# Performance work log

Hardware: AMD Instinct MI355X
Metric: run time of the kernel (lower is better)

The kernel has to match this reference:

```python
import jax, jax.numpy as jnp
import numpy as np
import math

B, S, D, H = 4, 2048, 512, 8
HD = D // H  # head dim = 64

def setup_inputs() -> dict:
    key = jax.random.key(0)
    ks = jax.random.split(key, 12)
    inp = {
        'queries': jax.random.normal(ks[0], (B, S, D), jnp.float32),
        'keys': jax.random.normal(ks[1], (B, S, D), jnp.float32),
        'values': jax.random.normal(ks[2], (B, S, D), jnp.float32),
        'valid_lens': jax.random.randint(ks[3], (B,), 0, 2048, jnp.int32),
        'Wq': jax.random.normal(ks[4], (D, D), jnp.float32) / math.sqrt(D),
        'bq': jnp.zeros((D,), jnp.float32),
        'Wk': jax.random.normal(ks[5], (D, D), jnp.float32) / math.sqrt(D),
        'bk': jnp.zeros((D,), jnp.float32),
        'Wv': jax.random.normal(ks[6], (D, D), jnp.float32) / math.sqrt(D),
        'bv': jnp.zeros((D,), jnp.float32),
        'Wo': jax.random.normal(ks[7], (D, D), jnp.float32) / math.sqrt(D),
        'bo': jnp.zeros((D,), jnp.float32),
    }
    return inp

def reference(queries, keys, values, valid_lens, Wq, bq, Wk, bk, Wv, bv, Wo, bo):
    # project and split heads: [B,S,D] -> [B,H,S,HD]
    def split_heads(x):
        return x.reshape(B, S, H, HD).transpose(0, 2, 1, 3)
    q = split_heads(queries @ Wq + bq)
    k = split_heads(keys @ Wk + bk)
    v = split_heads(values @ Wv + bv)
    # scores [B,H,Sq,Sk]
    scores = jnp.einsum('bhqd,bhkd->bhqk', q, k) / math.sqrt(HD)
    # masked softmax: mask key positions >= valid_len with -1e6 (d2l semantics)
    mask = jnp.arange(S)[None, None, None, :] < valid_lens[:, None, None, None]
    scores = jnp.where(mask, scores, -1e6)
    attn = jax.nn.softmax(scores, axis=-1)
    out = jnp.einsum('bhqk,bhkd->bhqd', attn, v)  # [B,H,S,HD]
    out = out.transpose(0, 2, 1, 3).reshape(B, S, D)
    return out @ Wo + bo
```

## Files before the change

### kernel.cpp

```cpp
#include <hip/hip_runtime.h>
#include <hip/hip_bf16.h>

typedef _Float16 half8 __attribute__((ext_vector_type(8)));
typedef _Float16 half4 __attribute__((ext_vector_type(4)));
typedef float floatx4 __attribute__((ext_vector_type(4)));
typedef float floatx16 __attribute__((ext_vector_type(16)));
typedef unsigned int uint2v __attribute__((ext_vector_type(2)));

#define LOG2E 1.44269504088896340736f

__device__ __forceinline__ half8 cvt8r(floatx4 a, floatx4 b) {
    half8 h;
    h[0] = (_Float16)a[0]; h[1] = (_Float16)a[1]; h[2] = (_Float16)a[2]; h[3] = (_Float16)a[3];
    h[4] = (_Float16)b[0]; h[5] = (_Float16)b[1]; h[6] = (_Float16)b[2]; h[7] = (_Float16)b[3];
    return h;
}

union H8U { half8 h; uint2v u[2]; };

__global__ __launch_bounds__(256) void transpose_w_kernel(
        const float* __restrict__ Wq, const float* __restrict__ Wk,
        const float* __restrict__ Wv, const float* __restrict__ Wo,
        _Float16* __restrict__ out) {
    const float* W = (blockIdx.z == 0) ? Wq : (blockIdx.z == 1) ? Wk : (blockIdx.z == 2) ? Wv : Wo;
    _Float16* o = out + (size_t)blockIdx.z * 512 * 512;
    __shared__ __align__(16) _Float16 t[64][72];
    int r0 = blockIdx.x * 64, c0 = blockIdx.y * 64;
    int tid = threadIdx.x;
    for (int i = 0; i < 2; i++) {
        int f = i * 256 + tid;
        int row = f >> 3, seg = f & 7;
        const float* p = W + (size_t)(r0 + row) * 512 + c0 + seg * 8;
        *(half8*)&t[row][seg * 8] = cvt8r(*(const floatx4*)p, *(const floatx4*)(p + 4));
    }
    __syncthreads();
    for (int i = 0; i < 2; i++) {
        int f = i * 256 + tid;
        int crow = f >> 3, seg = f & 7;
        half8 hv;
        for (int j = 0; j < 8; j++) hv[j] = t[seg * 8 + j][crow];
        *(half8*)(o + (size_t)(c0 + crow) * 512 + r0 + seg * 8) = hv;
    }
}

__global__ __launch_bounds__(256) void gemm_qkv_kernel(
        const float* __restrict__ Xq, const float* __restrict__ Xk, const float* __restrict__ Xv,
        const _Float16* __restrict__ WTall,
        const float* __restrict__ bq, const float* __restrict__ bk, const float* __restrict__ bv,
        const int* __restrict__ vlens,
        _Float16* __restrict__ qo, _Float16* __restrict__ ko2, _Float16* __restrict__ vto) {
    int z = blockIdx.z;
    int mBase = blockIdx.x * 64, nBase = blockIdx.y * 128;

    if (z >= 1) {
        int b_ = mBase >> 11, s0 = mBase & 2047;
        int L = vlens[b_];
        if (s0 >= L && !(z == 2 && L == 0)) return;
    }

    const float* X = (z == 0) ? Xq : (z == 1) ? Xk : Xv;
    const _Float16* BT = WTall + (size_t)z * 512 * 512;
    const float* bias = (z == 0) ? bq : (z == 1) ? bk : bv;

    __shared__ __align__(16) _Float16 Asm[64][72];
    __shared__ __align__(16) _Float16 Bsm[128][72];

    int tid = threadIdx.x;
    int wave = tid >> 6, lane = tid & 63;
    int lrow = lane & 15, quad = lane >> 4;
    int mrow = wave * 16 + lrow;

    const floatx4 fz = {0.f, 0.f, 0.f, 0.f};
    floatx4 acc[8];
    for (int i = 0; i < 8; i++) acc[i] = fz;

    int arow[2], aseg[2], brow[4], bseg[4];
    for (int i = 0; i < 2; i++) { int f = i * 256 + tid; arow[i] = f >> 3; aseg[i] = f & 7; }
    for (int i = 0; i < 4; i++) { int f = i * 256 + tid; brow[i] = f >> 3; bseg[i] = f & 7; }

    floatx4 areg[2][2];
    half8 breg[4];
    for (int i = 0; i < 2; i++) {
        const float* pa = X + (size_t)(mBase + arow[i]) * 512 + aseg[i] * 8;
        areg[i][0] = *(const floatx4*)pa;
        areg[i][1] = *(const floatx4*)(pa + 4);
    }
    for (int i = 0; i < 4; i++)
        breg[i] = *(const half8*)(BT + (size_t)(nBase + brow[i]) * 512 + bseg[i] * 8);

    for (int kb = 0; kb < 512; kb += 64) {
        for (int i = 0; i < 2; i++) *(half8*)&Asm[arow[i]][aseg[i] * 8] = cvt8r(areg[i][0], areg[i][1]);
        for (int i = 0; i < 4; i++) *(half8*)&Bsm[brow[i]][bseg[i] * 8] = breg[i];
        __syncthreads();
        if (kb + 64 < 512) {
            int kn = kb + 64;
            for (int i = 0; i < 2; i++) {
                const float* pa = X + (size_t)(mBase + arow[i]) * 512 + kn + aseg[i] * 8;
                areg[i][0] = *(const floatx4*)pa;
                areg[i][1] = *(const floatx4*)(pa + 4);
            }
            for (int i = 0; i < 4; i++)
                breg[i] = *(const half8*)(BT + (size_t)(nBase + brow[i]) * 512 + kn + bseg[i] * 8);
        }
        for (int kc = 0; kc < 2; kc++) {
            int ko_ = kc * 32 + quad * 8;
            half8 a = *(const half8*)&Asm[mrow][ko_];
            for (int nt = 0; nt < 8; nt++) {
                half8 b = *(const half8*)&Bsm[nt * 16 + lrow][ko_];
                acc[nt] = __builtin_amdgcn_mfma_f32_16x16x32_f16(a, b, acc[nt], 0, 0, 0);
            }
        }
        __syncthreads();
    }

    if (z == 2) {
        for (int nt = 0; nt < 8; nt++) {
            int gc = nBase + nt * 16 + lrow;
            float bb = bias[gc];
            int h = gc >> 6, hd = gc & 63;
            int gr = mBase + wave * 16 + quad * 4;
            int b_ = gr >> 11, s = gr & 2047;
            half4 hv;
            for (int r = 0; r < 4; r++) hv[r] = (_Float16)(acc[nt][r] + bb);
            *(half4*)(vto + (((size_t)(b_ * 8 + h) * 64 + hd) * 2048 + s)) = hv;
        }
    } else {
        _Float16* out = (z == 0) ? qo : ko2;
        for (int nt = 0; nt < 8; nt++) {
            int gc = nBase + nt * 16 + lrow;
            float bb = bias[gc];
            int h = gc >> 6, hd = gc & 63;
            for (int r = 0; r < 4; r++) {
                int gr = mBase + wave * 16 + quad * 4 + r;
                int b_ = gr >> 11, s = gr & 2047;
                out[(((size_t)b_ * 8 + h) * 2048 + s) * 64 + hd] = (_Float16)(acc[nt][r] + bb);
            }
        }
    }
}

__global__ __launch_bounds__(128) void attn_kernel(
        const _Float16* __restrict__ qws, const _Float16* __restrict__ kws,
        const _Float16* __restrict__ vtws, const int* __restrict__ vlens,
        _Float16* __restrict__ aout) {
    int idx = blockIdx.x;
    int b = ((idx & 3) + (idx >> 8)) & 3;
    int h = (idx >> 2) & 7;
    int q0 = ((idx >> 5) & 31) * 64;
    int bh = b * 8 + h;
    int L = vlens[b];
    bool uni = (L == 0);
    int nkt = uni ? 32 : ((L + 63) >> 6);
    int nfull = uni ? 0 : (L >> 6);

    int tid = threadIdx.x;
    int wq = tid >> 6;
    int lane = tid & 63;
    int l31 = lane & 31, hi = lane >> 5;

    __shared__ __align__(16) _Float16 ksm[64 * 64];
    __shared__ __align__(16) _Float16 vtsm[64 * 64];
    char* ksmB = (char*)ksm;
    char* vsmB = (char*)vtsm;

    const _Float16* kbase = kws + (size_t)bh * 2048 * 64;
    const _Float16* vtbase = vtws + (size_t)bh * 64 * 2048;

    half8 qf[4];
    {
        const _Float16* qrow = qws + ((size_t)bh * 2048 + q0 + wq * 32 + l31) * 64;
#pragma unroll
        for (int kc = 0; kc < 4; kc++) {
            qf[kc] = *(const half8*)(qrow + kc * 16 + hi * 8);
            qf[kc] = qf[kc] * (_Float16)(0.125f * LOG2E);
        }
    }

    floatx16 oacc0, oacc1;
#pragma unroll
    for (int i = 0; i < 16; i++) { oacc0[i] = 0.f; oacc1[i] = 0.f; }
    float rs = 0.f;

    int seg = tid & 7;
    int trow = tid >> 3;
    int xr = (l31 & 15) << 3;

    half8 kreg[4], vreg[4];
#pragma unroll
    for (int i = 0; i < 4; i++) {
        int row = i * 16 + trow;
        kreg[i] = *(const half8*)(kbase + row * 64 + seg * 8);
        vreg[i] = *(const half8*)(vtbase + (size_t)row * 2048 + seg * 8);
    }

    for (int kt = 0; kt < nkt; kt++) {
#pragma unroll
        for (int i = 0; i < 4; i++) {
            int row = i * 16 + trow;
            int wo = row * 128 + ((seg * 16) ^ ((row & 15) << 3));
            H8U kv, vv;
            kv.h = kreg[i]; vv.h = vreg[i];
            *(uint2v*)(ksmB + wo) = kv.u[0];
            *(uint2v*)(ksmB + (wo ^ 8)) = kv.u[1];
            *(uint2v*)(vsmB + wo) = vv.u[0];
            *(uint2v*)(vsmB + (wo ^ 8)) = vv.u[1];
        }
        __syncthreads();
        if (kt + 1 < nkt) {
            const _Float16* kn = kbase + (size_t)(kt + 1) * 4096;
            const _Float16* vn = vtbase + (kt + 1) * 64;
#pragma unroll
            for (int i = 0; i < 4; i++) {
                int row = i * 16 + trow;
                kreg[i] = *(const half8*)(kn + row * 64 + seg * 8);
                vreg[i] = *(const half8*)(vn + (size_t)row * 2048 + seg * 8);
            }
        }

#pragma unroll
        for (int t = 0; t < 2; t++) {
            floatx16 sacc;
#pragma unroll
            for (int i = 0; i < 16; i++) sacc[i] = 0.f;
            int rbase = (t * 32 + l31) * 128;
#pragma unroll
            for (int kc = 0; kc < 4; kc++) {
                int off = rbase + ((kc * 32 + hi * 16) ^ xr);
                H8U kf;
                kf.u[0] = *(const uint2v*)(ksmB + off);
                kf.u[1] = *(const uint2v*)(ksmB + (off ^ 8));
                sacc = __builtin_amdgcn_mfma_f32_32x32x16_f16(kf.h, qf[kc], sacc, 0, 0, 0);
            }

            float p[16];
            if (kt < nfull) {
#pragma unroll
                for (int r = 0; r < 16; r++) p[r] = exp2f(sacc[r]);
            } else {
                int kb0 = kt * 64 + t * 32 + 4 * hi;
#pragma unroll
                for (int r = 0; r < 16; r++) {
                    int key = kb0 + (r & 3) + 8 * (r >> 2);
                    p[r] = uni ? 1.0f : ((key < L) ? exp2f(sacc[r]) : 0.0f);
                }
            }
#pragma unroll
            for (int r = 0; r < 16; r++) rs += p[r];

#pragma unroll
            for (int s2 = 0; s2 < 2; s2++) {
                int s = t * 2 + s2;
                H8U pa;
#pragma unroll
                for (int j = 0; j < 8; j++) pa.h[j] = (_Float16)p[s2 * 8 + j];
                int cb = (s * 32 + hi * 8) ^ xr;
                {
                    int off = l31 * 128 + cb;
                    H8U vf;
                    vf.u[0] = *(const uint2v*)(vsmB + off);
                    vf.u[1] = *(const uint2v*)(vsmB + (off ^ 16));
                    oacc0 = __builtin_amdgcn_mfma_f32_32x32x16_f16(pa.h, vf.h, oacc0, 0, 0, 0);
                }
                {
                    int off = (32 + l31) * 128 + cb;
                    H8U vf;
                    vf.u[0] = *(const uint2v*)(vsmB + off);
                    vf.u[1] = *(const uint2v*)(vsmB + (off ^ 16));
                    oacc1 = __builtin_amdgcn_mfma_f32_32x32x16_f16(pa.h, vf.h, oacc1, 0, 0, 0);
                }
            }
        }
        __syncthreads();
    }

    float rstot = rs + __shfl_xor(rs, 32, 64);
    _Float16* outb = aout + ((size_t)b * 2048 + q0 + wq * 32) * 512 + h * 64;
#pragma unroll
    for (int r = 0; r < 16; r++) {
        int qi = (r & 3) + 8 * (r >> 2) + 4 * hi;
        float inv = 1.0f / __shfl(rstot, qi, 64);
        outb[(size_t)qi * 512 + l31] = (_Float16)(oacc0[r] * inv);
        outb[(size_t)qi * 512 + 32 + l31] = (_Float16)(oacc1[r] * inv);
    }
}

__global__ __launch_bounds__(256) void gemm_out_kernel(
        const _Float16* __restrict__ A, const _Float16* __restrict__ BT,
        const float* __restrict__ bias, float* __restrict__ out) {
    __shared__ __align__(16) _Float16 Asm[64][72];
    __shared__ __align__(16) _Float16 Bsm[128][72];

    int tid = threadIdx.x;
    int wave = tid >> 6, lane = tid & 63;
    int lrow = lane & 15, quad = lane >> 4;
    int mBase = blockIdx.x * 64, nBase = blockIdx.y * 128;
    int mrow = wave * 16 + lrow;

    const floatx4 fz = {0.f, 0.f, 0.f, 0.f};
    floatx4 acc[8];
    for (int i = 0; i < 8; i++) acc[i] = fz;

    int arow[2], aseg[2], brow[4], bseg[4];
    for (int i = 0; i < 2; i++) { int f = i * 256 + tid; arow[i] = f >> 3; aseg[i] = f & 7; }
    for (int i = 0; i < 4; i++) { int f = i * 256 + tid; brow[i] = f >> 3; bseg[i] = f & 7; }

    half8 areg[2], breg[4];
    for (int i = 0; i < 2; i++)
        areg[i] = *(const half8*)(A + (size_t)(mBase + arow[i]) * 512 + aseg[i] * 8);
    for (int i = 0; i < 4; i++)
        breg[i] = *(const half8*)(BT + (size_t)(nBase + brow[i]) * 512 + bseg[i] * 8);

    for (int kb = 0; kb < 512; kb += 64) {
        for (int i = 0; i < 2; i++) *(half8*)&Asm[arow[i]][aseg[i] * 8] = areg[i];
        for (int i = 0; i < 4; i++) *(half8*)&Bsm[brow[i]][bseg[i] * 8] = breg[i];
        __syncthreads();
        if (kb + 64 < 512) {
            int kn = kb + 64;
            for (int i = 0; i < 2; i++)
                areg[i] = *(const half8*)(A + (size_t)(mBase + arow[i]) * 512 + kn + aseg[i] * 8);
            for (int i = 0; i < 4; i++)
                breg[i] = *(const half8*)(BT + (size_t)(nBase + brow[i]) * 512 + kn + bseg[i] * 8);
        }
        for (int kc = 0; kc < 2; kc++) {
            int ko_ = kc * 32 + quad * 8;
            half8 a = *(const half8*)&Asm[mrow][ko_];
            for (int nt = 0; nt < 8; nt++) {
                half8 b = *(const half8*)&Bsm[nt * 16 + lrow][ko_];
                acc[nt] = __builtin_amdgcn_mfma_f32_16x16x32_f16(a, b, acc[nt], 0, 0, 0);
            }
        }
        __syncthreads();
    }

    for (int nt = 0; nt < 8; nt++) {
        int gc = nBase + nt * 16 + lrow;
        float bb = bias[gc];
        for (int r = 0; r < 4; r++) {
            int gr = mBase + wave * 16 + quad * 4 + r;
            out[(size_t)gr * 512 + gc] = acc[nt][r] + bb;
        }
    }
}

extern "C" void kernel_launch(void* const* d_in, const int* in_sizes, int n_in,
                              void* d_out, int out_size, void* d_ws, size_t ws_size,
                              hipStream_t stream) {
    const float* Q  = (const float*)d_in[0];
    const float* K  = (const float*)d_in[1];
    const float* V  = (const float*)d_in[2];
    const int*   VL = (const int*)d_in[3];
    const float* Wq = (const float*)d_in[4];
    const float* bq = (const float*)d_in[5];
    const float* Wk = (const float*)d_in[6];
    const float* bk = (const float*)d_in[7];
    const float* Wv = (const float*)d_in[8];
    const float* bv = (const float*)d_in[9];
    const float* Wo = (const float*)d_in[10];
    const float* bo = (const float*)d_in[11];

    char* ws = (char*)d_ws;
    _Float16* WT   = (_Float16*)ws;
    _Float16* qws  = (_Float16*)(ws + (size_t)(2)  * 1024 * 1024);
    _Float16* kws  = (_Float16*)(ws + (size_t)(10) * 1024 * 1024);
    _Float16* aout = (_Float16*)(ws + (size_t)(18) * 1024 * 1024);
    _Float16* vtws = (_Float16*)(ws + (size_t)(26) * 1024 * 1024);

    transpose_w_kernel<<<dim3(8, 8, 4), 256, 0, stream>>>(Wq, Wk, Wv, Wo, WT);
    gemm_qkv_kernel<<<dim3(128, 4, 3), 256, 0, stream>>>(Q, K, V, WT, bq, bk, bv, VL, qws, kws, vtws);
    attn_kernel<<<dim3(1024, 1, 1), 128, 0, stream>>>(qws, kws, vtws, VL, aout);
    gemm_out_kernel<<<dim3(128, 4, 1), 256, 0, stream>>>(aout, WT + (size_t)3 * 512 * 512, bo, (float*)d_out);
}
```

Baseline: 194.0 us.

## Double attention key tile to 128 with new LDS swizzle and packed conversions

The attention kernel now stages 128 keys per iteration instead of 64, which halves the number of barrier-separated loop trips. It also switches to a new XOR swizzle so K fragments load as single 16-byte LDS reads. P is converted with packed cvt_pkrtz, 32-key sub-tiles entirely beyond the valid length are skipped, and the row sums use tree reduction into two partial accumulators. In exchange it uses twice the LDS and twice the prefetch registers per block, which may lower occupancy.

```diff
diff --git a/kernel.cpp b/kernel.cpp
--- a/kernel.cpp
+++ b/kernel.cpp
@@ -3,6 +3,7 @@
 
 typedef _Float16 half8 __attribute__((ext_vector_type(8)));
 typedef _Float16 half4 __attribute__((ext_vector_type(4)));
+typedef _Float16 half2t __attribute__((ext_vector_type(2)));
 typedef float floatx4 __attribute__((ext_vector_type(4)));
 typedef float floatx16 __attribute__((ext_vector_type(16)));
 typedef unsigned int uint2v __attribute__((ext_vector_type(2)));
@@ -16,7 +17,11 @@
     return h;
 }
 
-union H8U { half8 h; uint2v u[2]; };
+union H8U { half8 h; half2t v2[4]; uint2v u[2]; };
+
+__device__ __forceinline__ half2t pk16(float a, float b) {
+    return __builtin_bit_cast(half2t, __builtin_amdgcn_cvt_pkrtz(a, b));
+}
 
 __global__ __launch_bounds__(256) void transpose_w_kernel(
         const float* __restrict__ Wq, const float* __restrict__ Wk,
@@ -150,16 +155,16 @@
     int bh = b * 8 + h;
     int L = vlens[b];
     bool uni = (L == 0);
-    int nkt = uni ? 32 : ((L + 63) >> 6);
-    int nfull = uni ? 0 : (L >> 6);
+    int nkt = uni ? 16 : ((L + 127) >> 7);
+    int nfull = uni ? 0 : (L >> 7);
 
     int tid = threadIdx.x;
     int wq = tid >> 6;
     int lane = tid & 63;
     int l31 = lane & 31, hi = lane >> 5;
 
-    __shared__ __align__(16) _Float16 ksm[64 * 64];
-    __shared__ __align__(16) _Float16 vtsm[64 * 64];
+    __shared__ __align__(16) _Float16 ksm[128 * 64];
+    __shared__ __align__(16) _Float16 vtsm[64 * 128];
     char* ksmB = (char*)ksm;
     char* vsmB = (char*)vtsm;
 
@@ -176,60 +181,54 @@
         }
     }
 
-    floatx16 oacc0, oacc1;
-#pragma unroll
-    for (int i = 0; i < 16; i++) { oacc0[i] = 0.f; oacc1[i] = 0.f; }
-    float rs = 0.f;
-
-    int seg = tid & 7;
-    int trow = tid >> 3;
-    int xr = (l31 & 15) << 3;
-
-    half8 kreg[4], vreg[4];
-#pragma unroll
-    for (int i = 0; i < 4; i++) {
-        int row = i * 16 + trow;
-        kreg[i] = *(const half8*)(kbase + row * 64 + seg * 8);
-        vreg[i] = *(const half8*)(vtbase + (size_t)row * 2048 + seg * 8);
+    floatx16 oc0, oc1;
+#pragma unroll
+    for (int i = 0; i < 16; i++) { oc0[i] = 0.f; oc1[i] = 0.f; }
+    float rsp0 = 0.f, rsp1 = 0.f;
+
+    int kthr = tid >> 3, ksg = tid & 7;
+    int vthr = tid >> 4, vsg = tid & 15;
+    int x15 = l31 & 15, x7 = l31 & 7;
+
+    half8 kreg[8], vreg[8];
+#pragma unroll
+    for (int i = 0; i < 8; i++) {
+        kreg[i] = *(const half8*)(kbase + (i * 16 + kthr) * 64 + ksg * 8);
+        vreg[i] = *(const half8*)(vtbase + (size_t)(i * 8 + vthr) * 2048 + vsg * 8);
     }
 
     for (int kt = 0; kt < nkt; kt++) {
 #pragma unroll
-        for (int i = 0; i < 4; i++) {
-            int row = i * 16 + trow;
-            int wo = row * 128 + ((seg * 16) ^ ((row & 15) << 3));
-            H8U kv, vv;
-            kv.h = kreg[i]; vv.h = vreg[i];
-            *(uint2v*)(ksmB + wo) = kv.u[0];
-            *(uint2v*)(ksmB + (wo ^ 8)) = kv.u[1];
-            *(uint2v*)(vsmB + wo) = vv.u[0];
-            *(uint2v*)(vsmB + (wo ^ 8)) = vv.u[1];
+        for (int i = 0; i < 8; i++) {
+            int kr = i * 16 + kthr;
+            *(half8*)(ksmB + kr * 128 + ((ksg ^ (kr & 7)) << 4)) = kreg[i];
+            int vr = i * 8 + vthr;
+            *(half8*)(vsmB + vr * 256 + ((vsg ^ (vr & 15)) << 4)) = vreg[i];
         }
         __syncthreads();
         if (kt + 1 < nkt) {
-            const _Float16* kn = kbase + (size_t)(kt + 1) * 4096;
-            const _Float16* vn = vtbase + (kt + 1) * 64;
-#pragma unroll
-            for (int i = 0; i < 4; i++) {
-                int row = i * 16 + trow;
-                kreg[i] = *(const half8*)(kn + row * 64 + seg * 8);
-                vreg[i] = *(const half8*)(vn + (size_t)row * 2048 + seg * 8);
-            }
-        }
-
-#pragma unroll
-        for (int t = 0; t < 2; t++) {
+            const _Float16* kn = kbase + (size_t)(kt + 1) * 128 * 64;
+            const _Float16* vn = vtbase + (kt + 1) * 128;
+#pragma unroll
+            for (int i = 0; i < 8; i++) {
+                kreg[i] = *(const half8*)(kn + (i * 16 + kthr) * 64 + ksg * 8);
+                vreg[i] = *(const half8*)(vn + (size_t)(i * 8 + vthr) * 2048 + vsg * 8);
+            }
+        }
+
+#pragma unroll
+        for (int t = 0; t < 4; t++) {
+            if (!uni && kt * 128 + t * 32 >= L) continue;
+
             floatx16 sacc;
 #pragma unroll
             for (int i = 0; i < 16; i++) sacc[i] = 0.f;
             int rbase = (t * 32 + l31) * 128;
 #pragma unroll
             for (int kc = 0; kc < 4; kc++) {
-                int off = rbase + ((kc * 32 + hi * 16) ^ xr);
-                H8U kf;
-                kf.u[0] = *(const uint2v*)(ksmB + off);
-                kf.u[1] = *(const uint2v*)(ksmB + (off ^ 8));
-                sacc = __builtin_amdgcn_mfma_f32_32x32x16_f16(kf.h, qf[kc], sacc, 0, 0, 0);
+                int c = 2 * kc + hi;
+                half8 kf = *(const half8*)(ksmB + rbase + ((c ^ x7) << 4));
+                sacc = __builtin_amdgcn_mfma_f32_32x32x16_f16(kf, qf[kc], sacc, 0, 0, 0);
             }
 
             float p[16];
@@ -237,50 +236,48 @@
 #pragma unroll
                 for (int r = 0; r < 16; r++) p[r] = exp2f(sacc[r]);
             } else {
-                int kb0 = kt * 64 + t * 32 + 4 * hi;
+                int kb0 = kt * 128 + t * 32 + 4 * hi;
 #pragma unroll
                 for (int r = 0; r < 16; r++) {
                     int key = kb0 + (r & 3) + 8 * (r >> 2);
                     p[r] = uni ? 1.0f : ((key < L) ? exp2f(sacc[r]) : 0.0f);
                 }
             }
-#pragma unroll
-            for (int r = 0; r < 16; r++) rs += p[r];
+            float ts = (((p[0] + p[1]) + (p[2] + p[3])) + ((p[4] + p[5]) + (p[6] + p[7])))
+                     + (((p[8] + p[9]) + (p[10] + p[11])) + ((p[12] + p[13]) + (p[14] + p[15])));
+            if (t & 1) rsp1 += ts; else rsp0 += ts;
 
 #pragma unroll
             for (int s2 = 0; s2 < 2; s2++) {
                 int s = t * 2 + s2;
                 H8U pa;
 #pragma unroll
-                for (int j = 0; j < 8; j++) pa.h[j] = (_Float16)p[s2 * 8 + j];
-                int cb = (s * 32 + hi * 8) ^ xr;
-                {
-                    int off = l31 * 128 + cb;
-                    H8U vf;
-                    vf.u[0] = *(const uint2v*)(vsmB + off);
-                    vf.u[1] = *(const uint2v*)(vsmB + (off ^ 16));
-                    oacc0 = __builtin_amdgcn_mfma_f32_32x32x16_f16(pa.h, vf.h, oacc0, 0, 0, 0);
-                }
-                {
-                    int off = (32 + l31) * 128 + cb;
-                    H8U vf;
-                    vf.u[0] = *(const uint2v*)(vsmB + off);
-                    vf.u[1] = *(const uint2v*)(vsmB + (off ^ 16));
-                    oacc1 = __builtin_amdgcn_mfma_f32_32x32x16_f16(pa.h, vf.h, oacc1, 0, 0, 0);
-                }
-            }
-        }
-        __syncthreads();
-    }
-
+                for (int jj = 0; jj < 4; jj++)
+                    pa.v2[jj] = pk16(p[s2 * 8 + jj * 2], p[s2 * 8 + jj * 2 + 1]);
+                int cA = (((2 * s) ^ x15) << 4) + 8 * hi;
+                int cB = (((2 * s + 1) ^ x15) << 4) + 8 * hi;
+                int ro0 = l31 * 256, ro1 = (32 + l31) * 256;
+                H8U vf0, vf1;
+                vf0.u[0] = *(const uint2v*)(vsmB + ro0 + cA);
+                vf0.u[1] = *(const uint2v*)(vsmB + ro0 + cB);
+                vf1.u[0] = *(const uint2v*)(vsmB + ro1 + cA);
+                vf1.u[1] = *(const uint2v*)(vsmB + ro1 + cB);
+                oc0 = __builtin_amdgcn_mfma_f32_32x32x16_f16(pa.h, vf0.h, oc0, 0, 0, 0);
+                oc1 = __builtin_amdgcn_mfma_f32_32x32x16_f16(pa.h, vf1.h, oc1, 0, 0, 0);
+            }
+        }
+        __syncthreads();
+    }
+
+    float rs = rsp0 + rsp1;
     float rstot = rs + __shfl_xor(rs, 32, 64);
     _Float16* outb = aout + ((size_t)b * 2048 + q0 + wq * 32) * 512 + h * 64;
 #pragma unroll
     for (int r = 0; r < 16; r++) {
         int qi = (r & 3) + 8 * (r >> 2) + 4 * hi;
         float inv = 1.0f / __shfl(rstot, qi, 64);
-        outb[(size_t)qi * 512 + l31] = (_Float16)(oacc0[r] * inv);
-        outb[(size_t)qi * 512 + 32 + l31] = (_Float16)(oacc1[r] * inv);
+        outb[(size_t)qi * 512 + l31] = (_Float16)(oc0[r] * inv);
+        outb[(size_t)qi * 512 + 32 + l31] = (_Float16)(oc1[r] * inv);
     }
 }
 
```

New measurement: 195.4 us. No clear change (+0.7%).

## Split attention key tiles across two wave pairs with LDS reduction

Applied to the files above, without the earlier changes.

The attention block grows from 128 to 256 threads. Each pair of waves processes alternating 64-key tiles, with each half of the block loading its own tile into a separate LDS buffer. The two partial output accumulators and row sums are then combined through shared memory before normalization. This doubles the waves working on each query block so latency is better hidden, at the cost of twice the LDS, an extra reduction step, and wasted work when the number of tiles is odd. The unused half2 union member appears to be leftover.

```diff
diff --git a/kernel.cpp b/kernel.cpp
--- a/kernel.cpp
+++ b/kernel.cpp
@@ -3,6 +3,7 @@
 
 typedef _Float16 half8 __attribute__((ext_vector_type(8)));
 typedef _Float16 half4 __attribute__((ext_vector_type(4)));
+typedef _Float16 half2t __attribute__((ext_vector_type(2)));
 typedef float floatx4 __attribute__((ext_vector_type(4)));
 typedef float floatx16 __attribute__((ext_vector_type(16)));
 typedef unsigned int uint2v __attribute__((ext_vector_type(2)));
@@ -16,7 +17,7 @@
     return h;
 }
 
-union H8U { half8 h; uint2v u[2]; };
+union H8U { half8 h; half2t v2[4]; uint2v u[2]; };
 
 __global__ __launch_bounds__(256) void transpose_w_kernel(
         const float* __restrict__ Wq, const float* __restrict__ Wk,
@@ -139,7 +140,7 @@
     }
 }
 
-__global__ __launch_bounds__(128) void attn_kernel(
+__global__ __launch_bounds__(256) void attn_kernel(
         const _Float16* __restrict__ qws, const _Float16* __restrict__ kws,
         const _Float16* __restrict__ vtws, const int* __restrict__ vlens,
         _Float16* __restrict__ aout) {
@@ -154,14 +155,13 @@
     int nfull = uni ? 0 : (L >> 6);
 
     int tid = threadIdx.x;
-    int wq = tid >> 6;
+    int wid = tid >> 6;
+    int wq = wid & 1, ks = wid >> 1;
     int lane = tid & 63;
     int l31 = lane & 31, hi = lane >> 5;
 
-    __shared__ __align__(16) _Float16 ksm[64 * 64];
-    __shared__ __align__(16) _Float16 vtsm[64 * 64];
-    char* ksmB = (char*)ksm;
-    char* vsmB = (char*)vtsm;
+    __shared__ __align__(16) _Float16 ksm[2][64 * 64];
+    __shared__ __align__(16) _Float16 vtsm[2][64 * 64];
 
     const _Float16* kbase = kws + (size_t)bh * 2048 * 64;
     const _Float16* vtbase = vtws + (size_t)bh * 64 * 2048;
@@ -181,106 +181,140 @@
     for (int i = 0; i < 16; i++) { oacc0[i] = 0.f; oacc1[i] = 0.f; }
     float rs = 0.f;
 
-    int seg = tid & 7;
-    int trow = tid >> 3;
+    int htid = tid & 127;
+    int tt = tid >> 7;
+    int seg = htid & 7;
+    int trow = htid >> 3;
     int xr = (l31 & 15) << 3;
+    char* ksmB = (char*)&ksm[tt][0];
+    char* vsmB = (char*)&vtsm[tt][0];
 
     half8 kreg[4], vreg[4];
-#pragma unroll
-    for (int i = 0; i < 4; i++) {
-        int row = i * 16 + trow;
-        kreg[i] = *(const half8*)(kbase + row * 64 + seg * 8);
-        vreg[i] = *(const half8*)(vtbase + (size_t)row * 2048 + seg * 8);
-    }
-
-    for (int kt = 0; kt < nkt; kt++) {
+    if (tt < nkt) {
+        const _Float16* kp = kbase + (size_t)tt * 4096;
+        const _Float16* vp = vtbase + tt * 64;
 #pragma unroll
         for (int i = 0; i < 4; i++) {
             int row = i * 16 + trow;
-            int wo = row * 128 + ((seg * 16) ^ ((row & 15) << 3));
-            H8U kv, vv;
-            kv.h = kreg[i]; vv.h = vreg[i];
-            *(uint2v*)(ksmB + wo) = kv.u[0];
-            *(uint2v*)(ksmB + (wo ^ 8)) = kv.u[1];
-            *(uint2v*)(vsmB + wo) = vv.u[0];
-            *(uint2v*)(vsmB + (wo ^ 8)) = vv.u[1];
-        }
-        __syncthreads();
-        if (kt + 1 < nkt) {
-            const _Float16* kn = kbase + (size_t)(kt + 1) * 4096;
-            const _Float16* vn = vtbase + (kt + 1) * 64;
+            kreg[i] = *(const half8*)(kp + row * 64 + seg * 8);
+            vreg[i] = *(const half8*)(vp + (size_t)row * 2048 + seg * 8);
+        }
+    }
+
+    for (int kt2 = 0; kt2 < nkt; kt2 += 2) {
+        if (kt2 + tt < nkt) {
 #pragma unroll
             for (int i = 0; i < 4; i++) {
                 int row = i * 16 + trow;
-                kreg[i] = *(const half8*)(kn + row * 64 + seg * 8);
-                vreg[i] = *(const half8*)(vn + (size_t)row * 2048 + seg * 8);
-            }
-        }
-
-#pragma unroll
-        for (int t = 0; t < 2; t++) {
-            floatx16 sacc;
-#pragma unroll
-            for (int i = 0; i < 16; i++) sacc[i] = 0.f;
-            int rbase = (t * 32 + l31) * 128;
-#pragma unroll
-            for (int kc = 0; kc < 4; kc++) {
-                int off = rbase + ((kc * 32 + hi * 16) ^ xr);
-                H8U kf;
-                kf.u[0] = *(const uint2v*)(ksmB + off);
-                kf.u[1] = *(const uint2v*)(ksmB + (off ^ 8));
-                sacc = __builtin_amdgcn_mfma_f32_32x32x16_f16(kf.h, qf[kc], sacc, 0, 0, 0);
-            }
-
-            float p[16];
-            if (kt < nfull) {
-#pragma unroll
-                for (int r = 0; r < 16; r++) p[r] = exp2f(sacc[r]);
-            } else {
-                int kb0 = kt * 64 + t * 32 + 4 * hi;
-#pragma unroll
-                for (int r = 0; r < 16; r++) {
-                    int key = kb0 + (r & 3) + 8 * (r >> 2);
-                    p[r] = uni ? 1.0f : ((key < L) ? exp2f(sacc[r]) : 0.0f);
+                int wo = row * 128 + ((seg * 16) ^ ((row & 15) << 3));
+                H8U kv, vv;
+                kv.h = kreg[i]; vv.h = vreg[i];
+                *(uint2v*)(ksmB + wo) = kv.u[0];
+                *(uint2v*)(ksmB + (wo ^ 8)) = kv.u[1];
+                *(uint2v*)(vsmB + wo) = vv.u[0];
+                *(uint2v*)(vsmB + (wo ^ 8)) = vv.u[1];
+            }
+        }
+        __syncthreads();
+        int nxt = kt2 + 2 + tt;
+        if (nxt < nkt) {
+            const _Float16* kp = kbase + (size_t)nxt * 4096;
+            const _Float16* vp = vtbase + nxt * 64;
+#pragma unroll
+            for (int i = 0; i < 4; i++) {
+                int row = i * 16 + trow;
+                kreg[i] = *(const half8*)(kp + row * 64 + seg * 8);
+                vreg[i] = *(const half8*)(vp + (size_t)row * 2048 + seg * 8);
+            }
+        }
+
+        int kt = kt2 + ks;
+        if (kt < nkt) {
+#pragma unroll
+            for (int t = 0; t < 2; t++) {
+                floatx16 sacc;
+#pragma unroll
+                for (int i = 0; i < 16; i++) sacc[i] = 0.f;
+                int rbase = (t * 32 + l31) * 128;
+#pragma unroll
+                for (int kc = 0; kc < 4; kc++) {
+                    int off = rbase + ((kc * 32 + hi * 16) ^ xr);
+                    H8U kf;
+                    kf.u[0] = *(const uint2v*)(ksmB + off);
+                    kf.u[1] = *(const uint2v*)(ksmB + (off ^ 8));
+                    sacc = __builtin_amdgcn_mfma_f32_32x32x16_f16(kf.h, qf[kc], sacc, 0, 0, 0);
                 }
-            }
-#pragma unroll
-            for (int r = 0; r < 16; r++) rs += p[r];
-
-#pragma unroll
-            for (int s2 = 0; s2 < 2; s2++) {
-                int s = t * 2 + s2;
-                H8U pa;
-#pragma unroll
-                for (int j = 0; j < 8; j++) pa.h[j] = (_Float16)p[s2 * 8 + j];
-                int cb = (s * 32 + hi * 8) ^ xr;
-                {
-                    int off = l31 * 128 + cb;
-                    H8U vf;
-                    vf.u[0] = *(const uint2v*)(vsmB + off);
-                    vf.u[1] = *(const uint2v*)(vsmB + (off ^ 16));
-                    oacc0 = __builtin_amdgcn_mfma_f32_32x32x16_f16(pa.h, vf.h, oacc0, 0, 0, 0);
+
+                float p[16];
+                if (kt < nfull) {
+#pragma unroll
+                    for (int r = 0; r < 16; r++) p[r] = exp2f(sacc[r]);
+                } else {
+                    int kb0 = kt * 64 + t * 32 + 4 * hi;
+#pragma unroll
+                    for (int r = 0; r < 16; r++) {
+                        int key = kb0 + (r & 3) + 8 * (r >> 2);
+                        p[r] = uni ? 1.0f : ((key < L) ? exp2f(sacc[r]) : 0.0f);
+                    }
                 }
-                {
-                    int off = (32 + l31) * 128 + cb;
-                    H8U vf;
-                    vf.u[0] = *(const uint2v*)(vsmB + off);
-                    vf.u[1] = *(const uint2v*)(vsmB + (off ^ 16));
-                    oacc1 = __builtin_amdgcn_mfma_f32_32x32x16_f16(pa.h, vf.h, oacc1, 0, 0, 0);
+#pragma unroll
+                for (int r = 0; r < 16; r++) rs += p[r];
+
+#pragma unroll
+                for (int s2 = 0; s2 < 2; s2++) {
+                    int s = t * 2 + s2;
+                    H8U pa;
+#pragma unroll
+                    for (int j = 0; j < 8; j++) pa.h[j] = (_Float16)p[s2 * 8 + j];
+                    int cb = (s * 32 + hi * 8) ^ xr;
+                    {
+                        int off = l31 * 128 + cb;
+                        H8U vf;
+                        vf.u[0] = *(const uint2v*)(vsmB + off);
+                        vf.u[1] = *(const uint2v*)(vsmB + (off ^ 16));
+                        oacc0 = __builtin_amdgcn_mfma_f32_32x32x16_f16(pa.h, vf.h, oacc0, 0, 0, 0);
+                    }
+                    {
+                        int off = (32 + l31) * 128 + cb;
+                        H8U vf;
+                        vf.u[0] = *(const uint2v*)(vsmB + off);
+                        vf.u[1] = *(const uint2v*)(vsmB + (off ^ 16));
+                        oacc1 = __builtin_amdgcn_mfma_f32_32x32x16_f16(pa.h, vf.h, oacc1, 0, 0, 0);
+                    }
                 }
             }
         }
         __syncthreads();
     }
 
-    float rstot = rs + __shfl_xor(rs, 32, 64);
-    _Float16* outb = aout + ((size_t)b * 2048 + q0 + wq * 32) * 512 + h * 64;
-#pragma unroll
-    for (int r = 0; r < 16; r++) {
-        int qi = (r & 3) + 8 * (r >> 2) + 4 * hi;
-        float inv = 1.0f / __shfl(rstot, qi, 64);
-        outb[(size_t)qi * 512 + l31] = (_Float16)(oacc0[r] * inv);
-        outb[(size_t)qi * 512 + 32 + l31] = (_Float16)(oacc1[r] * inv);
+    float* ocs = (float*)&ksm[0][0];
+    float* rss = (float*)&vtsm[0][0];
+    if (ks == 1) {
+        int sb = wq * 2048;
+        rss[wq * 64 + lane] = rs;
+#pragma unroll
+        for (int i = 0; i < 16; i++) ocs[sb + i * 64 + lane] = oacc0[i];
+#pragma unroll
+        for (int i = 0; i < 16; i++) ocs[sb + (16 + i) * 64 + lane] = oacc1[i];
+    }
+    __syncthreads();
+    if (ks == 0) {
+        int sb = wq * 2048;
+        rs += rss[wq * 64 + lane];
+#pragma unroll
+        for (int i = 0; i < 16; i++) oacc0[i] += ocs[sb + i * 64 + lane];
+#pragma unroll
+        for (int i = 0; i < 16; i++) oacc1[i] += ocs[sb + (16 + i) * 64 + lane];
+
+        float rstot = rs + __shfl_xor(rs, 32, 64);
+        _Float16* outb = aout + ((size_t)b * 2048 + q0 + wq * 32) * 512 + h * 64;
+#pragma unroll
+        for (int r = 0; r < 16; r++) {
+            int qi = (r & 3) + 8 * (r >> 2) + 4 * hi;
+            float inv = 1.0f / __shfl(rstot, qi, 64);
+            outb[(size_t)qi * 512 + l31] = (_Float16)(oacc0[r] * inv);
+            outb[(size_t)qi * 512 + 32 + l31] = (_Float16)(oacc1[r] * inv);
+        }
     }
 }
 
@@ -367,6 +401,6 @@
 
     transpose_w_kernel<<<dim3(8, 8, 4), 256, 0, stream>>>(Wq, Wk, Wv, Wo, WT);
     gemm_qkv_kernel<<<dim3(128, 4, 3), 256, 0, stream>>>(Q, K, V, WT, bq, bk, bv, VL, qws, kws, vtws);
-    attn_kernel<<<dim3(1024, 1, 1), 128, 0, stream>>>(qws, kws, vtws, VL, aout);
+    attn_kernel<<<dim3(1024, 1, 1), 256, 0, stream>>>(qws, kws, vtws, VL, aout);
     gemm_out_kernel<<<dim3(128, 4, 1), 256, 0, stream>>>(aout, WT + (size_t)3 * 512 * 512, bo, (float*)d_out);
 }
```

Measured after the change: 192.6 us. About the same (-0.7%).
